# Kernel tuning notes

Hardware: AMD Instinct MI355X
Metric: run time of the kernel (lower is better)

The kernel has to match this reference:

```python
import jax, jax.numpy as jnp
import numpy as np

# EISANI constants (inference path, dense non-EI weights, static connections)
NUM_BITS = 16        # EISANITABcontinuousVarEncodingNumBits
K_SYN = 32           # numberOfSynapsesPerSegment
SEGMENTS = 2         # numberOfSegmentsPerNeuron
THETA = 8            # segment activation threshold (synapse-count based)
H = 4096             # hiddenLayerSize
F = 128              # numberOfFeatures
C = 10               # numberOfClasses
B = 64               # batch


def _make_weight(key, h, s, p):
    """Dense weight [h, s, p] with exactly K_SYN nonzero +/-1 synapses per segment
    (mirrors _initialise_layer_weights dense non-EI branch)."""
    k1, k2 = jax.random.split(key)
    cols = jax.random.randint(k1, (h, s, K_SYN), 0, p)
    signs = jnp.where(jax.random.bernoulli(k2, 0.5, (h, s, K_SYN)), 1.0, -1.0).astype(jnp.float32)
    hh = jnp.arange(h)[:, None, None]
    ss = jnp.arange(s)[None, :, None]
    return jnp.zeros((h, s, p), jnp.float32).at[hh, ss, cols].set(signs)


def setup_inputs() -> dict:
    key = jax.random.key(0)
    kx, k0, k1, k2, ko = jax.random.split(key, 5)
    x = jax.random.uniform(kx, (B, F), dtype=jnp.float32)
    W0 = _make_weight(k0, H, SEGMENTS, F * NUM_BITS)
    W1 = _make_weight(k1, H, SEGMENTS, H)
    W2 = _make_weight(k2, H, SEGMENTS, H)
    outW = jax.random.normal(ko, (3, H, C), dtype=jnp.float32) * 0.02
    return {"x": x, "W0": W0, "W1": W1, "W2": W2, "outW": outW}


def _encode(x):
    # thermometer (graded) encoding of continuous vars into NUM_BITS binary bits
    thresholds = (jnp.arange(NUM_BITS, dtype=jnp.float32) + 1.0) / (NUM_BITS + 1.0)
    bits = (x[:, :, None] >= thresholds).astype(jnp.float32)  # [B, F, NUM_BITS]
    return bits.reshape(x.shape[0], -1)  # [B, F*NUM_BITS]


def reference(x, W0, W1, W2, outW):
    acts = _encode(x)  # [B, P0]
    layer_acts = []
    for W in (W0, W1, W2):
        # segment membrane sums over binary presynaptic activations
        z = jnp.einsum('bp,hsp->bhs', acts, W)  # [B, H, S]
        # neuron fires if ANY segment reaches threshold
        fired = jnp.any(z >= THETA, axis=-1)
        acts = fired.astype(jnp.float32)  # binary activation [B, H]
        layer_acts.append(acts)
    stacked = jnp.stack(layer_acts)  # [L, B, H]
    out = jnp.einsum('lbh,lhc->bc', stacked, outW)  # class scores [B, C]
    return out
```

## Files before the change

### kernel.cpp

```cpp
#include <hip/hip_runtime.h>
#include <hip/hip_bf16.h>

typedef unsigned long long u64;

#define H_SZ 4096
#define NBITS 16
#define NFEAT 128
#define NCLS 10
#define THETA 8


__global__ void encode_kernel(const float* __restrict__ x, u64* __restrict__ actp0) {
    int idx = blockIdx.x * blockDim.x + threadIdx.x;
    if (idx >= 32 * 64) return;
    int wword = idx >> 6;
    int b = idx & 63;
    int c = wword >> 2, j = wword & 3;
    u64 word = 0;
    for (int i = 0; i < 64; i++) {
        int p = c * 256 + 4 * i + j;
        int f = p >> 4, t = p & 15;
        float thr = (t + 1.0f) / (NBITS + 1.0f);
        if (x[b * NFEAT + f] >= thr) word |= (1ULL << i);
    }
    actp0[wword * 64 + b] = word;
}

template <int P>
__global__ __launch_bounds__(256) void layer_kernel(const float* __restrict__ W,
                                                    const u64* __restrict__ actp,
                                                    u64* __restrict__ ballots) {
    constexpr int NW = P / 64;
    __shared__ u64 lds[NW * 64];
    int tid = threadIdx.x;
    for (int i = tid; i < NW * 64; i += 256) lds[i] = actp[i];
    __syncthreads();

    int lane = tid & 63;
    int warp = tid >> 6;
    #pragma unroll
    for (int r = 0; r < 2; r++) {
        int wid = (blockIdx.x * 4 + warp) * 2 + r;
        const float4* wrow = (const float4*)(W + (size_t)wid * P) + lane;
        unsigned int zp = 0, zn = 0;
        #pragma unroll
        for (int c = 0; c < P / 256; c++) {
            float4 w = wrow[c * 64];
            u64 p0 = __ballot(w.x > 0.0f);
            u64 n0 = __ballot(w.x < 0.0f);
            u64 p1 = __ballot(w.y > 0.0f);
            u64 n1 = __ballot(w.y < 0.0f);
            u64 p2 = __ballot(w.z > 0.0f);
            u64 n2 = __ballot(w.z < 0.0f);
            u64 p3 = __ballot(w.w > 0.0f);
            u64 n3 = __ballot(w.w < 0.0f);
            u64 a0 = lds[(c * 4 + 0) * 64 + lane];
            u64 a1 = lds[(c * 4 + 1) * 64 + lane];
            u64 a2 = lds[(c * 4 + 2) * 64 + lane];
            u64 a3 = lds[(c * 4 + 3) * 64 + lane];
            zp += __builtin_popcountll(a0 & p0) + __builtin_popcountll(a1 & p1)
                + __builtin_popcountll(a2 & p2) + __builtin_popcountll(a3 & p3);
            zn += __builtin_popcountll(a0 & n0) + __builtin_popcountll(a1 & n1)
                + __builtin_popcountll(a2 & n2) + __builtin_popcountll(a3 & n3);
        }
        int z = (int)zp - (int)zn;
        u64 fz = __ballot(z >= THETA);
        if (lane == 0) ballots[wid] = fz;
    }
}

__global__ void transpose_kernel(const u64* __restrict__ ballots,
                                 u64* __restrict__ f,
                                 u64* __restrict__ actp) {
    __shared__ u64 lds[256];
    int c = blockIdx.x;
    int tid = threadIdx.x;
    int h = c * 256 + tid;
    u64 fh = ballots[2 * h] | ballots[2 * h + 1];
    f[h] = fh;
    lds[tid] = fh;
    __syncthreads();
    int j = tid >> 6, b = tid & 63;
    u64 word = 0;
    #pragma unroll 8
    for (int i = 0; i < 64; i++)
        word |= ((lds[4 * i + j] >> b) & 1ULL) << i;
    actp[(c * 4 + j) * 64 + b] = word;
}

__global__ void output_kernel(const float* __restrict__ outW,
                              const u64* __restrict__ f,
                              float* __restrict__ out) {
    int tid = threadIdx.x;
    int lane = tid & 63;
    int wid = blockIdx.x * 4 + (tid >> 6);
    int l = wid / (NCLS * 64);
    int rem = wid % (NCLS * 64);
    int c = rem / 64;
    int chunk = rem % 64;
    const u64* fl = f + l * H_SZ;
    int h0 = chunk * 64;
    float acc = 0.0f;
    #pragma unroll 8
    for (int h = h0; h < h0 + 64; h++) {
        float wv = outW[((size_t)(l * H_SZ + h)) * NCLS + c];
        u64 ball = fl[h];
        if ((ball >> lane) & 1ULL) acc += wv;
    }
    atomicAdd(&out[lane * NCLS + c], acc);
}

extern "C" void kernel_launch(void* const* d_in, const int* in_sizes, int n_in,
                              void* d_out, int out_size, void* d_ws, size_t ws_size,
                              hipStream_t stream) {
    const float* x    = (const float*)d_in[0];
    const float* W0   = (const float*)d_in[1];
    const float* W1   = (const float*)d_in[2];
    const float* W2   = (const float*)d_in[3];
    const float* outW = (const float*)d_in[4];
    float* out = (float*)d_out;

    char* ws = (char*)d_ws;
    u64* actp0   = (u64*)(ws);
    u64* actp1   = (u64*)(ws + 16384);
    u64* actp2   = (u64*)(ws + 49152);
    u64* ballots = (u64*)(ws + 81920);
    u64* f       = (u64*)(ws + 147456);
    u64* scratch = (u64*)(ws + 245760);

    hipMemsetAsync(d_out, 0, (size_t)out_size * sizeof(float), stream);

    encode_kernel<<<8, 256, 0, stream>>>(x, actp0);

    layer_kernel<2048><<<1024, 256, 0, stream>>>(W0, actp0, ballots);
    transpose_kernel<<<16, 256, 0, stream>>>(ballots, f + 0 * H_SZ, actp1);

    layer_kernel<4096><<<1024, 256, 0, stream>>>(W1, actp1, ballots);
    transpose_kernel<<<16, 256, 0, stream>>>(ballots, f + 1 * H_SZ, actp2);

    layer_kernel<4096><<<1024, 256, 0, stream>>>(W2, actp2, ballots);
    transpose_kernel<<<16, 256, 0, stream>>>(ballots, f + 2 * H_SZ, scratch);

    output_kernel<<<480, 256, 0, stream>>>(outW, f, out);
}
```

Baseline: 394.3 us.

## Use nontemporal weight loads, interleave two rows, fuse last transpose into output

The layer kernel now processes both weight rows of a wave in one loop, sharing the LDS activation loads and using nontemporal float4 loads. It also raises the occupancy hint in launch bounds and copies activations into LDS as 16-byte vectors. The final transpose launch is removed, and the output kernel reads the layer-3 ballots directly. The encode kernel is restructured to reuse each input load across four thresholds. The intent is to cut streaming cost on the dense weights and remove one launch, at the price of higher register pressure.

```diff
diff --git a/kernel.cpp b/kernel.cpp
--- a/kernel.cpp
+++ b/kernel.cpp
@@ -2,6 +2,7 @@
 #include <hip/hip_bf16.h>
 
 typedef unsigned long long u64;
+typedef float f32x4 __attribute__((ext_vector_type(4)));
 
 #define H_SZ 4096
 #define NBITS 16
@@ -16,56 +17,78 @@
     int wword = idx >> 6;
     int b = idx & 63;
     int c = wword >> 2, j = wword & 3;
+    float thr0 = (4 * 0 + j + 1.0f) / (NBITS + 1.0f);
+    float thr1 = (4 * 1 + j + 1.0f) / (NBITS + 1.0f);
+    float thr2 = (4 * 2 + j + 1.0f) / (NBITS + 1.0f);
+    float thr3 = (4 * 3 + j + 1.0f) / (NBITS + 1.0f);
+    const float* xb = x + b * NFEAT + c * 16;
     u64 word = 0;
-    for (int i = 0; i < 64; i++) {
-        int p = c * 256 + 4 * i + j;
-        int f = p >> 4, t = p & 15;
-        float thr = (t + 1.0f) / (NBITS + 1.0f);
-        if (x[b * NFEAT + f] >= thr) word |= (1ULL << i);
+    #pragma unroll
+    for (int k = 0; k < 16; k++) {
+        float xv = xb[k];
+        word |= (u64)(xv >= thr0) << (4 * k + 0);
+        word |= (u64)(xv >= thr1) << (4 * k + 1);
+        word |= (u64)(xv >= thr2) << (4 * k + 2);
+        word |= (u64)(xv >= thr3) << (4 * k + 3);
     }
     actp0[wword * 64 + b] = word;
 }
 
 template <int P>
-__global__ __launch_bounds__(256) void layer_kernel(const float* __restrict__ W,
-                                                    const u64* __restrict__ actp,
-                                                    u64* __restrict__ ballots) {
+__global__ __launch_bounds__(256, 4) void layer_kernel(const float* __restrict__ W,
+                                                       const u64* __restrict__ actp,
+                                                       u64* __restrict__ ballots) {
     constexpr int NW = P / 64;
-    __shared__ u64 lds[NW * 64];
+    __shared__ __align__(16) u64 lds[NW * 64];
     int tid = threadIdx.x;
-    for (int i = tid; i < NW * 64; i += 256) lds[i] = actp[i];
+    const ulonglong2* src = (const ulonglong2*)actp;
+    ulonglong2* dst = (ulonglong2*)lds;
+    #pragma unroll
+    for (int i = tid; i < NW * 32; i += 256) dst[i] = src[i];
     __syncthreads();
 
     int lane = tid & 63;
     int warp = tid >> 6;
-    #pragma unroll
-    for (int r = 0; r < 2; r++) {
-        int wid = (blockIdx.x * 4 + warp) * 2 + r;
-        const float4* wrow = (const float4*)(W + (size_t)wid * P) + lane;
-        unsigned int zp = 0, zn = 0;
-        #pragma unroll
-        for (int c = 0; c < P / 256; c++) {
-            float4 w = wrow[c * 64];
-            u64 p0 = __ballot(w.x > 0.0f);
-            u64 n0 = __ballot(w.x < 0.0f);
-            u64 p1 = __ballot(w.y > 0.0f);
-            u64 n1 = __ballot(w.y < 0.0f);
-            u64 p2 = __ballot(w.z > 0.0f);
-            u64 n2 = __ballot(w.z < 0.0f);
-            u64 p3 = __ballot(w.w > 0.0f);
-            u64 n3 = __ballot(w.w < 0.0f);
-            u64 a0 = lds[(c * 4 + 0) * 64 + lane];
-            u64 a1 = lds[(c * 4 + 1) * 64 + lane];
-            u64 a2 = lds[(c * 4 + 2) * 64 + lane];
-            u64 a3 = lds[(c * 4 + 3) * 64 + lane];
-            zp += __builtin_popcountll(a0 & p0) + __builtin_popcountll(a1 & p1)
-                + __builtin_popcountll(a2 & p2) + __builtin_popcountll(a3 & p3);
-            zn += __builtin_popcountll(a0 & n0) + __builtin_popcountll(a1 & n1)
-                + __builtin_popcountll(a2 & n2) + __builtin_popcountll(a3 & n3);
-        }
-        int z = (int)zp - (int)zn;
-        u64 fz = __ballot(z >= THETA);
-        if (lane == 0) ballots[wid] = fz;
+    int wid0 = (blockIdx.x * 4 + warp) * 2;
+    const f32x4* w0 = (const f32x4*)(W + (size_t)wid0 * P) + lane;
+    const f32x4* w1 = (const f32x4*)(W + (size_t)(wid0 + 1) * P) + lane;
+
+    unsigned int zp0 = 0, zn0 = 0, zp1 = 0, zn1 = 0;
+    #pragma unroll 4
+    for (int c = 0; c < P / 256; c++) {
+        f32x4 a = __builtin_nontemporal_load(w0 + c * 64);
+        f32x4 b = __builtin_nontemporal_load(w1 + c * 64);
+        u64 A0 = lds[(c * 4 + 0) * 64 + lane];
+        u64 A1 = lds[(c * 4 + 1) * 64 + lane];
+        u64 A2 = lds[(c * 4 + 2) * 64 + lane];
+        u64 A3 = lds[(c * 4 + 3) * 64 + lane];
+
+        u64 m;
+        m = __ballot(a.x > 0.0f); zp0 += __builtin_popcountll(A0 & m);
+        m = __ballot(a.x < 0.0f); zn0 += __builtin_popcountll(A0 & m);
+        m = __ballot(a.y > 0.0f); zp0 += __builtin_popcountll(A1 & m);
+        m = __ballot(a.y < 0.0f); zn0 += __builtin_popcountll(A1 & m);
+        m = __ballot(a.z > 0.0f); zp0 += __builtin_popcountll(A2 & m);
+        m = __ballot(a.z < 0.0f); zn0 += __builtin_popcountll(A2 & m);
+        m = __ballot(a.w > 0.0f); zp0 += __builtin_popcountll(A3 & m);
+        m = __ballot(a.w < 0.0f); zn0 += __builtin_popcountll(A3 & m);
+
+        m = __ballot(b.x > 0.0f); zp1 += __builtin_popcountll(A0 & m);
+        m = __ballot(b.x < 0.0f); zn1 += __builtin_popcountll(A0 & m);
+        m = __ballot(b.y > 0.0f); zp1 += __builtin_popcountll(A1 & m);
+        m = __ballot(b.y < 0.0f); zn1 += __builtin_popcountll(A1 & m);
+        m = __ballot(b.z > 0.0f); zp1 += __builtin_popcountll(A2 & m);
+        m = __ballot(b.z < 0.0f); zn1 += __builtin_popcountll(A2 & m);
+        m = __ballot(b.w > 0.0f); zp1 += __builtin_popcountll(A3 & m);
+        m = __ballot(b.w < 0.0f); zn1 += __builtin_popcountll(A3 & m);
+    }
+    int z0 = (int)zp0 - (int)zn0;
+    int z1 = (int)zp1 - (int)zn1;
+    u64 f0 = __ballot(z0 >= THETA);
+    u64 f1 = __ballot(z1 >= THETA);
+    if (lane == 0) {
+        ballots[wid0] = f0;
+        ballots[wid0 + 1] = f1;
     }
 }
 
@@ -90,6 +113,7 @@
 
 __global__ void output_kernel(const float* __restrict__ outW,
                               const u64* __restrict__ f,
+                              const u64* __restrict__ ballots,
                               float* __restrict__ out) {
     int tid = threadIdx.x;
     int lane = tid & 63;
@@ -98,14 +122,22 @@
     int rem = wid % (NCLS * 64);
     int c = rem / 64;
     int chunk = rem % 64;
-    const u64* fl = f + l * H_SZ;
     int h0 = chunk * 64;
     float acc = 0.0f;
-    #pragma unroll 8
-    for (int h = h0; h < h0 + 64; h++) {
-        float wv = outW[((size_t)(l * H_SZ + h)) * NCLS + c];
-        u64 ball = fl[h];
-        if ((ball >> lane) & 1ULL) acc += wv;
+    if (l < 2) {
+        const u64* fl = f + l * H_SZ;
+        #pragma unroll 8
+        for (int h = h0; h < h0 + 64; h++) {
+            float wv = outW[((size_t)(l * H_SZ + h)) * NCLS + c];
+            if ((fl[h] >> lane) & 1ULL) acc += wv;
+        }
+    } else {
+        #pragma unroll 8
+        for (int h = h0; h < h0 + 64; h++) {
+            float wv = outW[((size_t)(2 * H_SZ + h)) * NCLS + c];
+            u64 ball = ballots[2 * h] | ballots[2 * h + 1];
+            if ((ball >> lane) & 1ULL) acc += wv;
+        }
     }
     atomicAdd(&out[lane * NCLS + c], acc);
 }
@@ -126,7 +158,6 @@
     u64* actp2   = (u64*)(ws + 49152);
     u64* ballots = (u64*)(ws + 81920);
     u64* f       = (u64*)(ws + 147456);
-    u64* scratch = (u64*)(ws + 245760);
 
     hipMemsetAsync(d_out, 0, (size_t)out_size * sizeof(float), stream);
 
@@ -139,7 +170,6 @@
     transpose_kernel<<<16, 256, 0, stream>>>(ballots, f + 1 * H_SZ, actp2);
 
     layer_kernel<4096><<<1024, 256, 0, stream>>>(W2, actp2, ballots);
-    transpose_kernel<<<16, 256, 0, stream>>>(ballots, f + 2 * H_SZ, scratch);
 
-    output_kernel<<<480, 256, 0, stream>>>(outW, f, out);
+    output_kernel<<<480, 256, 0, stream>>>(outW, f, ballots, out);
 }
```

Result: faster. 365.7 us (-7.2%).
